# Performance work log

Measured on AMD Instinct MI355X. Metric: run time of the kernel, lower is better.

## Reference

```python
import jax, jax.numpy as jnp
import numpy as np

B, D_IMG, D_TXT, E = 4096, 768, 768, 512
LAMBDA_CMP = 1.0
EPS = 1e-10


def setup_inputs() -> dict:
    key = jax.random.key(0)
    k1, k2, k3, k4, k5 = jax.random.split(key, 5)
    return {
        "images": jax.random.normal(k1, (B, D_IMG), dtype=jnp.float32),
        "texts": jax.random.normal(k2, (B, D_TXT), dtype=jnp.float32),
        "labels": jax.random.randint(k3, (B,), 0, 1000, dtype=jnp.int32),
        "W_img": jax.random.normal(k4, (D_IMG, E), dtype=jnp.float32) / np.sqrt(D_IMG),
        "W_txt": jax.random.normal(k5, (D_TXT, E), dtype=jnp.float32) / np.sqrt(D_TXT),
        "logit_scale": jnp.asarray(np.log(1.0 / 0.07), dtype=jnp.float32),
    }


def reference(images, texts, labels, W_img, W_txt, logit_scale):
    # CLIP-style encoders: linear project + L2 normalize
    img = images @ W_img
    txt = texts @ W_txt
    img = img / jnp.linalg.norm(img, axis=-1, keepdims=True)
    txt = txt / jnp.linalg.norm(txt, axis=-1, keepdims=True)
    logits = jnp.exp(logit_scale) * (img @ txt.T)  # [B, B]

    b = logits.shape[0]
    rows = jnp.arange(b)
    logp = jax.nn.log_softmax(logits, axis=-1)
    clip_loss = -jnp.mean(logp[rows, labels])

    probs = jnp.exp(logp)                # softmax probs [B, B]
    p_yi = probs[rows, labels]           # [B]
    # columns j whose label differs from sample i's label AND prob exceeds p_yi
    diff_label = labels[None, :] != labels[:, None]           # [B, B]
    mask = diff_label & (probs > p_yi[:, None])               # [B, B]
    denom = jnp.sum(jnp.where(mask, probs, 0.0), axis=1)      # [B]
    has_any = jnp.any(mask, axis=1)
    cmp_loss = jnp.sum(jnp.where(has_any, p_yi / (denom + EPS), 0.0)) / b

    return clip_loss + LAMBDA_CMP * cmp_loss
```

## Files before the change

### kernel.cpp

```cpp
#include <hip/hip_runtime.h>
#include <stdint.h>

#define BATCH 4096
#define DDIM  768
#define EDIM  512
#define NSPLIT 16
#define LOG2E 1.44269504088896340736f

using short8  = __attribute__((ext_vector_type(8))) short;
using float4v = __attribute__((ext_vector_type(4))) float;

__device__ __forceinline__ unsigned short f2bf(float x) {
    union { float f; uint32_t u; } v; v.f = x;
    uint32_t u = v.u;
    u += 0x7FFFu + ((u >> 16) & 1u);
    return (unsigned short)(u >> 16);
}
__device__ __forceinline__ float bf2f(unsigned short h) {
    union { uint32_t u; float f; } v; v.u = ((uint32_t)h) << 16;
    return v.f;
}

__device__ __forceinline__ void gl2lds16(const void* g, void* l) {
    __builtin_amdgcn_global_load_lds(
        (const __attribute__((address_space(1))) void*)g,
        (__attribute__((address_space(3))) void*)l, 16, 0, 0);
}

__global__ void prep(const float* __restrict__ images, const float* __restrict__ texts,
                     const float* __restrict__ W_img, const float* __restrict__ W_txt,
                     unsigned short* __restrict__ img_bf, unsigned short* __restrict__ txt_bf,
                     unsigned short* __restrict__ wt_img, unsigned short* __restrict__ wt_txt) {
    __shared__ float tile[32][33];
    int bid = blockIdx.x;
    if (bid < 6144) {
        int which = bid >= 3072;
        int i = (bid - (which ? 3072 : 0)) * 256 + threadIdx.x;
        const float* in = which ? texts : images;
        unsigned short* out = which ? txt_bf : img_bf;
        float4 v = ((const float4*)in)[i];
        ushort4 o;
        o.x = f2bf(v.x); o.y = f2bf(v.y); o.z = f2bf(v.z); o.w = f2bf(v.w);
        ((ushort4*)out)[i] = o;
        return;
    }
    int tb = bid - 6144;
    int which = tb >= 384;
    if (which) tb -= 384;
    const float* W = which ? W_txt : W_img;
    unsigned short* Wt = which ? wt_txt : wt_img;
    int n0 = (tb & 15) * 32, k0 = (tb >> 4) * 32;
    int tid = threadIdx.x;
    for (int p = 0; p < 4; ++p) {
        int e = tid + p * 256; int lr = e >> 5, lc = e & 31;
        tile[lc][lr] = W[(size_t)(k0 + lr) * EDIM + n0 + lc];
    }
    __syncthreads();
    for (int p = 0; p < 4; ++p) {
        int e = tid + p * 256; int lr = e >> 5, lc = e & 31;
        Wt[(size_t)(n0 + lr) * DDIM + k0 + lc] = f2bf(tile[lr][lc]);
    }
}

__global__ __launch_bounds__(256) void gemm_nt(const unsigned short* __restrict__ Aimg,
                                               const unsigned short* __restrict__ Atxt,
                                               const unsigned short* __restrict__ Bimg,
                                               const unsigned short* __restrict__ Btxt,
                                               unsigned short* __restrict__ Cimg,
                                               unsigned short* __restrict__ Ctxt) {
    const unsigned short* A  = blockIdx.z ? Atxt : Aimg;
    const unsigned short* Bm = blockIdx.z ? Btxt : Bimg;
    unsigned short* C        = blockIdx.z ? Ctxt : Cimg;
    __shared__ __align__(16) unsigned short As[2][128 * 64];
    __shared__ __align__(16) unsigned short Bs[2][64 * 64];
    int tid = threadIdx.x;
    int wave = tid >> 6, lane = tid & 63;
    int q = lane >> 4, r = lane & 15;
    int m0 = blockIdx.x * 128, n0 = blockIdx.y * 64;
    int sw = (r >> 1) & 3;

    const unsigned short* gsA[4];
    unsigned short* lsA[4];
    for (int i = 0; i < 4; ++i) {
        int u = i * 256 + tid;
        int kc2 = u >> 9, row = (u >> 2) & 127, kq = u & 3;
        int kq2 = kq ^ ((row >> 1) & 3);
        gsA[i] = &A[(size_t)(m0 + row) * DDIM + kc2 * 32 + kq2 * 8];
        lsA[i] = &As[0][u * 8];
    }
    const unsigned short* gsB[2];
    unsigned short* lsB[2];
    for (int i = 0; i < 2; ++i) {
        int u = i * 256 + tid;
        int kc2 = u >> 8, row = (u >> 2) & 63, kq = u & 3;
        int kq2 = kq ^ ((row >> 1) & 3);
        gsB[i] = &Bm[(size_t)(n0 + row) * DDIM + kc2 * 32 + kq2 * 8];
        lsB[i] = &Bs[0][u * 8];
    }

    float4v acc[2][4];
    for (int a = 0; a < 2; ++a)
        for (int t = 0; t < 4; ++t) acc[a][t] = (float4v){0.f, 0.f, 0.f, 0.f};

    for (int i = 0; i < 4; ++i) gl2lds16(gsA[i], lsA[i]);
    for (int i = 0; i < 2; ++i) gl2lds16(gsB[i], lsB[i]);
    __syncthreads();

    for (int it = 0; it < DDIM / 64; ++it) {
        int b = it & 1;
        if (it < DDIM / 64 - 1) {
            int k0 = (it + 1) * 64;
            for (int i = 0; i < 4; ++i) gl2lds16(gsA[i] + k0, lsA[i] + (b ^ 1) * (128 * 64));
            for (int i = 0; i < 2; ++i) gl2lds16(gsB[i] + k0, lsB[i] + (b ^ 1) * (64 * 64));
        }
        for (int kc2 = 0; kc2 < 2; ++kc2) {
            short8 a0 = *(const short8*)&As[b][kc2 * 4096 + (wave * 32 + r) * 32 + (q ^ sw) * 8];
            short8 a1 = *(const short8*)&As[b][kc2 * 4096 + (wave * 32 + 16 + r) * 32 + (q ^ sw) * 8];
            for (int t = 0; t < 4; ++t) {
                short8 bfr = *(const short8*)&Bs[b][kc2 * 2048 + (t * 16 + r) * 32 + (q ^ sw) * 8];
                acc[0][t] = __builtin_amdgcn_mfma_f32_16x16x32_bf16(a0, bfr, acc[0][t], 0, 0, 0);
                acc[1][t] = __builtin_amdgcn_mfma_f32_16x16x32_bf16(a1, bfr, acc[1][t], 0, 0, 0);
            }
        }
        __syncthreads();
    }
    for (int rg = 0; rg < 2; ++rg)
        for (int t = 0; t < 4; ++t)
            for (int g = 0; g < 4; ++g)
                C[(size_t)(m0 + wave * 32 + rg * 16 + q * 4 + g) * EDIM + n0 + t * 16 + r] =
                    f2bf(acc[rg][t][g]);
}

__global__ void norm_rows(unsigned short* __restrict__ Pa, unsigned short* __restrict__ Pb) {
    unsigned short* P = blockIdx.y ? Pb : Pa;
    int wave = threadIdx.x >> 6, lane = threadIdx.x & 63;
    int row = blockIdx.x * 4 + wave;
    unsigned short* p = &P[(size_t)row * 512 + lane * 8];
    union { unsigned short us[8]; uint4 u4; } v;
    v.u4 = *(const uint4*)p;
    float f[8], s = 0.f;
    for (int j = 0; j < 8; ++j) { f[j] = bf2f(v.us[j]); s += f[j] * f[j]; }
    for (int off = 1; off < 64; off <<= 1) s += __shfl_xor(s, off);
    float rn = rsqrtf(s);
    for (int j = 0; j < 8; ++j) v.us[j] = f2bf(f[j] * rn);
    *(uint4*)p = v.u4;
}

__global__ void tdot(const unsigned short* __restrict__ img, const unsigned short* __restrict__ txt,
                     const int* __restrict__ labels, float* __restrict__ tout) {
    int wave = threadIdx.x >> 6, lane = threadIdx.x & 63;
    int row = blockIdx.x * 4 + wave;
    int lab = labels[row];
    union { unsigned short us[8]; uint4 u4; } a, b;
    a.u4 = *(const uint4*)&img[(size_t)row * 512 + lane * 8];
    b.u4 = *(const uint4*)&txt[(size_t)lab * 512 + lane * 8];
    float s = 0.f;
    for (int j = 0; j < 8; ++j) s += bf2f(a.us[j]) * bf2f(b.us[j]);
    for (int off = 1; off < 64; off <<= 1) s += __shfl_xor(s, off);
    if (lane == 0) tout[row] = s;
}

__global__ __launch_bounds__(512) void flash_pass(
    const unsigned short* __restrict__ img, const unsigned short* __restrict__ txt,
    const int* __restrict__ labels, const float* __restrict__ tvals,
    const float* __restrict__ ls,
    float* __restrict__ lP, float* __restrict__ dP) {
    __shared__ __align__(16) unsigned short Bs[2][16384];
    int tid = threadIdx.x;
    int wave = tid >> 6, lane = tid & 63;
    int q = lane >> 4, r = lane & 15;
    int split = blockIdx.x;
    int row0 = blockIdx.y * 128 + wave * 16;
    float alpha = expf(ls[0]);
    float c1 = alpha * LOG2E;

    int srow = (tid >> 2) & 63, kcb = tid >> 8, skp = tid & 3;
    int skp2 = skp ^ ((srow >> 1) & 3);
    int sw = (r >> 1) & 3;

    const unsigned short* gB0 = &txt[(size_t)(split * 256 + srow) * 512 + kcb * 32 + skp2 * 8];
    unsigned short* ld0 = &Bs[0][0] + (size_t)tid * 8;

    for (int i = 0; i < 4; ++i) gl2lds16(gB0 + i * 64, ld0 + i * 4096);

    short8 af[16];
    for (int kc = 0; kc < 16; ++kc)
        af[kc] = *(const short8*)&img[(size_t)(row0 + r) * 512 + kc * 32 + q * 8];

    int labr[4]; float tr[4];
    for (int g = 0; g < 4; ++g) {
        int rw = row0 + q * 4 + g;
        labr[g] = labels[rw];
        tr[g] = tvals[rw];
    }
    float l[4] = {0.f, 0.f, 0.f, 0.f}, d[4] = {0.f, 0.f, 0.f, 0.f};
    float4v acc[4];
    for (int t = 0; t < 4; ++t) acc[t] = (float4v){0.f, 0.f, 0.f, 0.f};

    __syncthreads();

    for (int s = 0; s < 8; ++s) {
        int buf = s & 1, h = s & 1;
        if (s < 7) {
            int sn = s + 1;
            const unsigned short* g = gB0 + (sn >> 1) * (64 * 512) + (sn & 1) * 256;
            unsigned short* ld = ld0 + (sn & 1) * 16384;
            for (int i = 0; i < 4; ++i) gl2lds16(g + i * 64, ld + i * 4096);
        }
        for (int kc = 0; kc < 8; ++kc) {
            short8 a = af[h * 8 + kc];
            for (int t = 0; t < 4; ++t) {
                short8 bfr = *(const short8*)&Bs[buf][(kc * 64 + t * 16 + r) * 32 + (q ^ sw) * 8];
                acc[t] = __builtin_amdgcn_mfma_f32_16x16x32_bf16(a, bfr, acc[t], 0, 0, 0);
            }
        }
        if (h == 1) {
            int colbase = split * 256 + (s >> 1) * 64;
            for (int t = 0; t < 4; ++t) {
                int lc = labels[colbase + t * 16 + r];
                for (int g = 0; g < 4; ++g) {
                    float a = acc[t][g];
                    float p = exp2f(fmaf(a, c1, -c1));
                    l[g] += p;
                    d[g] += ((a > tr[g]) && (lc != labr[g])) ? p : 0.f;
                }
            }
            for (int t = 0; t < 4; ++t) acc[t] = (float4v){0.f, 0.f, 0.f, 0.f};
        }
        __syncthreads();
    }
    for (int g = 0; g < 4; ++g) {
        float lv = l[g], dv = d[g];
        for (int off = 1; off < 16; off <<= 1) {
            lv += __shfl_xor(lv, off);
            dv += __shfl_xor(dv, off);
        }
        if (r == 0) {
            int rw = row0 + q * 4 + g;
            lP[(size_t)rw * NSPLIT + split] = lv;
            dP[(size_t)rw * NSPLIT + split] = dv;
        }
    }
}

__global__ void combine(const float* __restrict__ lP, const float* __restrict__ dP,
                        const float* __restrict__ tvals, const float* __restrict__ ls,
                        float* __restrict__ out) {
    int row = blockIdx.x * 256 + threadIdx.x;
    float alpha = expf(ls[0]);
    float L = 0.f, D = 0.f;
    for (int s = 0; s < NSPLIT; ++s) {
        L += lP[(size_t)row * NSPLIT + s];
        D += dP[(size_t)row * NSPLIT + s];
    }
    float tm = alpha * (tvals[row] - 1.0f);
    float clip = logf(L) - tm;
    float py = expf(tm) / L;
    float cmp = (D > 0.f) ? py / (D / L + 1e-10f) : 0.f;
    float v = clip + cmp;
    for (int off = 1; off < 64; off <<= 1) v += __shfl_xor(v, off);
    __shared__ float w4[4];
    int wave = threadIdx.x >> 6, lane = threadIdx.x & 63;
    if (lane == 0) w4[wave] = v;
    __syncthreads();
    if (threadIdx.x == 0)
        atomicAdd(out, (w4[0] + w4[1] + w4[2] + w4[3]) * (1.0f / BATCH));
}

extern "C" void kernel_launch(void* const* d_in, const int* in_sizes, int n_in,
                              void* d_out, int out_size, void* d_ws, size_t ws_size,
                              hipStream_t stream) {
    const float* images = (const float*)d_in[0];
    const float* texts  = (const float*)d_in[1];
    const int*   labels = (const int*)d_in[2];
    const float* W_img  = (const float*)d_in[3];
    const float* W_txt  = (const float*)d_in[4];
    const float* lscale = (const float*)d_in[5];
    float* out = (float*)d_out;

    char* ws = (char*)d_ws;
    unsigned short* img_bf = (unsigned short*)(ws + 0);
    unsigned short* txt_bf = (unsigned short*)(ws + 6291456);
    unsigned short* wt_img = (unsigned short*)(ws + 12582912);
    unsigned short* wt_txt = (unsigned short*)(ws + 13369344);
    unsigned short* proj_i = (unsigned short*)(ws + 14155776);
    unsigned short* proj_t = (unsigned short*)(ws + 18350080);
    float*          lP     = (float*)(ws + 0);
    float*          dP     = (float*)(ws + 262144);
    float*          tvals  = (float*)(ws + 524288);

    hipMemsetAsync(out, 0, sizeof(float), stream);
    prep<<<6912, 256, 0, stream>>>(images, texts, W_img, W_txt, img_bf, txt_bf, wt_img, wt_txt);
    gemm_nt<<<dim3(BATCH / 128, EDIM / 64, 2), 256, 0, stream>>>(img_bf, txt_bf, wt_img, wt_txt,
                                                                 proj_i, proj_t);
    norm_rows<<<dim3(BATCH / 4, 2), 256, 0, stream>>>(proj_i, proj_t);
    tdot<<<BATCH / 4, 256, 0, stream>>>(proj_i, proj_t, labels, tvals);
    flash_pass<<<dim3(NSPLIT, BATCH / 128), 512, 0, stream>>>(proj_i, proj_t, labels, tvals,
                                                              lscale, lP, dP);
    combine<<<16, 256, 0, stream>>>(lP, dP, tvals, lscale, out);
}
```

Before: 136.5 us.

## Give each flash_pass wave two 16-row tiles and halve block threads

The flash_pass kernel now runs 4 waves per block instead of 8, and each wave covers 32 image rows as two 16-row MFMA subtiles. Every B fragment read from LDS feeds two MFMAs, which halves LDS read traffic per MFMA. The txt tile loader is reorganised so 256 threads issue 8 global-to-LDS copies each. The cost is more registers per wave (doubled A fragments and accumulators) and fewer waves available to hide latency, which launch_bounds(256,2) tries to balance.

```diff
diff --git a/kernel.cpp b/kernel.cpp
--- a/kernel.cpp
+++ b/kernel.cpp
@@ -160,7 +160,7 @@
     if (lane == 0) tout[row] = s;
 }
 
-__global__ __launch_bounds__(512) void flash_pass(
+__global__ __launch_bounds__(256, 2) void flash_pass(
     const unsigned short* __restrict__ img, const unsigned short* __restrict__ txt,
     const int* __restrict__ labels, const float* __restrict__ tvals,
     const float* __restrict__ ls,
@@ -170,32 +170,36 @@
     int wave = tid >> 6, lane = tid & 63;
     int q = lane >> 4, r = lane & 15;
     int split = blockIdx.x;
-    int row0 = blockIdx.y * 128 + wave * 16;
+    int row0 = blockIdx.y * 128 + wave * 32;
     float alpha = expf(ls[0]);
     float c1 = alpha * LOG2E;
 
-    int srow = (tid >> 2) & 63, kcb = tid >> 8, skp = tid & 3;
+    int srow = (tid >> 2) & 63, skp = tid & 3;
     int skp2 = skp ^ ((srow >> 1) & 3);
     int sw = (r >> 1) & 3;
 
-    const unsigned short* gB0 = &txt[(size_t)(split * 256 + srow) * 512 + kcb * 32 + skp2 * 8];
+    const unsigned short* gB0 = &txt[(size_t)(split * 256 + srow) * 512 + skp2 * 8];
     unsigned short* ld0 = &Bs[0][0] + (size_t)tid * 8;
 
-    for (int i = 0; i < 4; ++i) gl2lds16(gB0 + i * 64, ld0 + i * 4096);
-
-    short8 af[16];
-    for (int kc = 0; kc < 16; ++kc)
-        af[kc] = *(const short8*)&img[(size_t)(row0 + r) * 512 + kc * 32 + q * 8];
-
-    int labr[4]; float tr[4];
-    for (int g = 0; g < 4; ++g) {
-        int rw = row0 + q * 4 + g;
-        labr[g] = labels[rw];
-        tr[g] = tvals[rw];
-    }
-    float l[4] = {0.f, 0.f, 0.f, 0.f}, d[4] = {0.f, 0.f, 0.f, 0.f};
-    float4v acc[4];
-    for (int t = 0; t < 4; ++t) acc[t] = (float4v){0.f, 0.f, 0.f, 0.f};
+    for (int i = 0; i < 8; ++i) gl2lds16(gB0 + i * 32, ld0 + i * 2048);
+
+    short8 af[2][16];
+    for (int st = 0; st < 2; ++st)
+        for (int kc = 0; kc < 16; ++kc)
+            af[st][kc] = *(const short8*)&img[(size_t)(row0 + st * 16 + r) * 512 + kc * 32 + q * 8];
+
+    int labr[2][4]; float tr[2][4];
+    for (int st = 0; st < 2; ++st)
+        for (int g = 0; g < 4; ++g) {
+            int rw = row0 + st * 16 + q * 4 + g;
+            labr[st][g] = labels[rw];
+            tr[st][g] = tvals[rw];
+        }
+    float l[2][4] = {{0.f, 0.f, 0.f, 0.f}, {0.f, 0.f, 0.f, 0.f}};
+    float d[2][4] = {{0.f, 0.f, 0.f, 0.f}, {0.f, 0.f, 0.f, 0.f}};
+    float4v acc[2][4];
+    for (int st = 0; st < 2; ++st)
+        for (int t = 0; t < 4; ++t) acc[st][t] = (float4v){0.f, 0.f, 0.f, 0.f};
 
     __syncthreads();
 
@@ -205,42 +209,46 @@
             int sn = s + 1;
             const unsigned short* g = gB0 + (sn >> 1) * (64 * 512) + (sn & 1) * 256;
             unsigned short* ld = ld0 + (sn & 1) * 16384;
-            for (int i = 0; i < 4; ++i) gl2lds16(g + i * 64, ld + i * 4096);
+            for (int i = 0; i < 8; ++i) gl2lds16(g + i * 32, ld + i * 2048);
         }
         for (int kc = 0; kc < 8; ++kc) {
-            short8 a = af[h * 8 + kc];
+            short8 a0 = af[0][h * 8 + kc];
+            short8 a1 = af[1][h * 8 + kc];
             for (int t = 0; t < 4; ++t) {
                 short8 bfr = *(const short8*)&Bs[buf][(kc * 64 + t * 16 + r) * 32 + (q ^ sw) * 8];
-                acc[t] = __builtin_amdgcn_mfma_f32_16x16x32_bf16(a, bfr, acc[t], 0, 0, 0);
+                acc[0][t] = __builtin_amdgcn_mfma_f32_16x16x32_bf16(a0, bfr, acc[0][t], 0, 0, 0);
+                acc[1][t] = __builtin_amdgcn_mfma_f32_16x16x32_bf16(a1, bfr, acc[1][t], 0, 0, 0);
             }
         }
         if (h == 1) {
             int colbase = split * 256 + (s >> 1) * 64;
             for (int t = 0; t < 4; ++t) {
                 int lc = labels[colbase + t * 16 + r];
-                for (int g = 0; g < 4; ++g) {
-                    float a = acc[t][g];
-                    float p = exp2f(fmaf(a, c1, -c1));
-                    l[g] += p;
-                    d[g] += ((a > tr[g]) && (lc != labr[g])) ? p : 0.f;
-                }
-            }
-            for (int t = 0; t < 4; ++t) acc[t] = (float4v){0.f, 0.f, 0.f, 0.f};
+                for (int st = 0; st < 2; ++st)
+                    for (int g = 0; g < 4; ++g) {
+                        float a = acc[st][t][g];
+                        float p = exp2f(fmaf(a, c1, -c1));
+                        l[st][g] += p;
+                        d[st][g] += ((a > tr[st][g]) && (lc != labr[st][g])) ? p : 0.f;
+                    }
+                for (int st = 0; st < 2; ++st) acc[st][t] = (float4v){0.f, 0.f, 0.f, 0.f};
+            }
         }
         __syncthreads();
     }
-    for (int g = 0; g < 4; ++g) {
-        float lv = l[g], dv = d[g];
-        for (int off = 1; off < 16; off <<= 1) {
-            lv += __shfl_xor(lv, off);
-            dv += __shfl_xor(dv, off);
-        }
-        if (r == 0) {
-            int rw = row0 + q * 4 + g;
-            lP[(size_t)rw * NSPLIT + split] = lv;
-            dP[(size_t)rw * NSPLIT + split] = dv;
-        }
-    }
+    for (int st = 0; st < 2; ++st)
+        for (int g = 0; g < 4; ++g) {
+            float lv = l[st][g], dv = d[st][g];
+            for (int off = 1; off < 16; off <<= 1) {
+                lv += __shfl_xor(lv, off);
+                dv += __shfl_xor(dv, off);
+            }
+            if (r == 0) {
+                int rw = row0 + st * 16 + q * 4 + g;
+                lP[(size_t)rw * NSPLIT + split] = lv;
+                dP[(size_t)rw * NSPLIT + split] = dv;
+            }
+        }
 }
 
 __global__ void combine(const float* __restrict__ lP, const float* __restrict__ dP,
@@ -295,7 +303,7 @@
                                                                  proj_i, proj_t);
     norm_rows<<<dim3(BATCH / 4, 2), 256, 0, stream>>>(proj_i, proj_t);
     tdot<<<BATCH / 4, 256, 0, stream>>>(proj_i, proj_t, labels, tvals);
-    flash_pass<<<dim3(NSPLIT, BATCH / 128), 512, 0, stream>>>(proj_i, proj_t, labels, tvals,
+    flash_pass<<<dim3(NSPLIT, BATCH / 128), 256, 0, stream>>>(proj_i, proj_t, labels, tvals,
                                                               lscale, lP, dP);
     combine<<<16, 256, 0, stream>>>(lP, dP, tvals, lscale, out);
 }
```

Result: slower. 157.8 us (+15.6%).

## Restructure similarity pass into 128x128 tiled GEMM with per-tile partial sums

Applied to the files above, without the earlier changes.

The flash pass changes from one block per 128 rows sweeping 256 columns, with the A operand held in registers and only 4 accumulators per wave, to a classic 128x128 output tile. Each block double-buffers both A and B K-slices into LDS, and each wave computes a 64x64 sub-tile (4x4 MFMA accumulators). The softmax and mask partial sums are then reduced per 64-column chunk, which raises the partial count per row from 16 to 64. The aim is more MFMA work per LDS fragment load and a larger grid (1024 blocks). The cost is extra A traffic through LDS and a larger partial buffer that combine must read.

```diff
diff --git a/kernel.cpp b/kernel.cpp
--- a/kernel.cpp
+++ b/kernel.cpp
@@ -4,7 +4,7 @@
 #define BATCH 4096
 #define DDIM  768
 #define EDIM  512
-#define NSPLIT 16
+#define NS    64
 #define LOG2E 1.44269504088896340736f
 
 using short8  = __attribute__((ext_vector_type(8))) short;
@@ -160,85 +160,106 @@
     if (lane == 0) tout[row] = s;
 }
 
-__global__ __launch_bounds__(512) void flash_pass(
+__global__ __launch_bounds__(256) void flash_pass(
     const unsigned short* __restrict__ img, const unsigned short* __restrict__ txt,
     const int* __restrict__ labels, const float* __restrict__ tvals,
     const float* __restrict__ ls,
     float* __restrict__ lP, float* __restrict__ dP) {
-    __shared__ __align__(16) unsigned short Bs[2][16384];
+    __shared__ __align__(16) unsigned short As[2][128 * 64];
+    __shared__ __align__(16) unsigned short Bs[2][128 * 64];
     int tid = threadIdx.x;
     int wave = tid >> 6, lane = tid & 63;
+    int wr = wave >> 1, wc = wave & 1;
     int q = lane >> 4, r = lane & 15;
-    int split = blockIdx.x;
-    int row0 = blockIdx.y * 128 + wave * 16;
+    int n0 = blockIdx.x * 128;
+    int m0 = blockIdx.y * 128;
     float alpha = expf(ls[0]);
     float c1 = alpha * LOG2E;
-
-    int srow = (tid >> 2) & 63, kcb = tid >> 8, skp = tid & 3;
-    int skp2 = skp ^ ((srow >> 1) & 3);
     int sw = (r >> 1) & 3;
 
-    const unsigned short* gB0 = &txt[(size_t)(split * 256 + srow) * 512 + kcb * 32 + skp2 * 8];
-    unsigned short* ld0 = &Bs[0][0] + (size_t)tid * 8;
-
-    for (int i = 0; i < 4; ++i) gl2lds16(gB0 + i * 64, ld0 + i * 4096);
-
-    short8 af[16];
-    for (int kc = 0; kc < 16; ++kc)
-        af[kc] = *(const short8*)&img[(size_t)(row0 + r) * 512 + kc * 32 + q * 8];
-
-    int labr[4]; float tr[4];
-    for (int g = 0; g < 4; ++g) {
-        int rw = row0 + q * 4 + g;
-        labr[g] = labels[rw];
-        tr[g] = tvals[rw];
-    }
-    float l[4] = {0.f, 0.f, 0.f, 0.f}, d[4] = {0.f, 0.f, 0.f, 0.f};
-    float4v acc[4];
-    for (int t = 0; t < 4; ++t) acc[t] = (float4v){0.f, 0.f, 0.f, 0.f};
-
+    const unsigned short* gsA[4]; const unsigned short* gsB[4];
+    unsigned short *lsA[4], *lsB[4];
+    for (int i = 0; i < 4; ++i) {
+        int u = i * 256 + tid;
+        int kc2 = u >> 9, row = (u >> 2) & 127, kq = u & 3;
+        int kq2 = kq ^ ((row >> 1) & 3);
+        gsA[i] = &img[(size_t)(m0 + row) * 512 + kc2 * 32 + kq2 * 8];
+        gsB[i] = &txt[(size_t)(n0 + row) * 512 + kc2 * 32 + kq2 * 8];
+        lsA[i] = &As[0][u * 8];
+        lsB[i] = &Bs[0][u * 8];
+    }
+
+    float4v acc[4][4];
+    #pragma unroll
+    for (int st = 0; st < 4; ++st)
+        #pragma unroll
+        for (int cf = 0; cf < 4; ++cf) acc[st][cf] = (float4v){0.f, 0.f, 0.f, 0.f};
+
+    for (int i = 0; i < 4; ++i) gl2lds16(gsA[i], lsA[i]);
+    for (int i = 0; i < 4; ++i) gl2lds16(gsB[i], lsB[i]);
     __syncthreads();
 
-    for (int s = 0; s < 8; ++s) {
-        int buf = s & 1, h = s & 1;
-        if (s < 7) {
-            int sn = s + 1;
-            const unsigned short* g = gB0 + (sn >> 1) * (64 * 512) + (sn & 1) * 256;
-            unsigned short* ld = ld0 + (sn & 1) * 16384;
-            for (int i = 0; i < 4; ++i) gl2lds16(g + i * 64, ld + i * 4096);
-        }
-        for (int kc = 0; kc < 8; ++kc) {
-            short8 a = af[h * 8 + kc];
-            for (int t = 0; t < 4; ++t) {
-                short8 bfr = *(const short8*)&Bs[buf][(kc * 64 + t * 16 + r) * 32 + (q ^ sw) * 8];
-                acc[t] = __builtin_amdgcn_mfma_f32_16x16x32_bf16(a, bfr, acc[t], 0, 0, 0);
+    for (int it = 0; it < 8; ++it) {
+        int b = it & 1;
+        if (it < 7) {
+            int k0 = (it + 1) * 64;
+            for (int i = 0; i < 4; ++i) gl2lds16(gsA[i] + k0, lsA[i] + (b ^ 1) * (128 * 64));
+            for (int i = 0; i < 4; ++i) gl2lds16(gsB[i] + k0, lsB[i] + (b ^ 1) * (128 * 64));
+        }
+        #pragma unroll
+        for (int kc2 = 0; kc2 < 2; ++kc2) {
+            short8 av[4], bv[4];
+            #pragma unroll
+            for (int st = 0; st < 4; ++st)
+                av[st] = *(const short8*)&As[b][kc2 * 4096 + (wr * 64 + st * 16 + r) * 32 + (q ^ sw) * 8];
+            #pragma unroll
+            for (int cf = 0; cf < 4; ++cf)
+                bv[cf] = *(const short8*)&Bs[b][kc2 * 4096 + (wc * 64 + cf * 16 + r) * 32 + (q ^ sw) * 8];
+            #pragma unroll
+            for (int st = 0; st < 4; ++st)
+                #pragma unroll
+                for (int cf = 0; cf < 4; ++cf)
+                    acc[st][cf] = __builtin_amdgcn_mfma_f32_16x16x32_bf16(av[st], bv[cf],
+                                                                          acc[st][cf], 0, 0, 0);
+        }
+        __syncthreads();
+    }
+
+    int lc[4];
+    #pragma unroll
+    for (int cf = 0; cf < 4; ++cf) lc[cf] = labels[n0 + wc * 64 + cf * 16 + r];
+    int cb = blockIdx.x * 2 + wc;
+    #pragma unroll
+    for (int st = 0; st < 4; ++st) {
+        int labr[4]; float tr[4];
+        #pragma unroll
+        for (int g = 0; g < 4; ++g) {
+            int rw = m0 + wr * 64 + st * 16 + q * 4 + g;
+            labr[g] = labels[rw];
+            tr[g] = tvals[rw];
+        }
+        float l4[4] = {0.f, 0.f, 0.f, 0.f}, d4[4] = {0.f, 0.f, 0.f, 0.f};
+        #pragma unroll
+        for (int cf = 0; cf < 4; ++cf)
+            #pragma unroll
+            for (int g = 0; g < 4; ++g) {
+                float a = acc[st][cf][g];
+                float p = exp2f(fmaf(a, c1, -c1));
+                l4[g] += p;
+                d4[g] += ((a > tr[g]) && (lc[cf] != labr[g])) ? p : 0.f;
             }
-        }
-        if (h == 1) {
-            int colbase = split * 256 + (s >> 1) * 64;
-            for (int t = 0; t < 4; ++t) {
-                int lc = labels[colbase + t * 16 + r];
-                for (int g = 0; g < 4; ++g) {
-                    float a = acc[t][g];
-                    float p = exp2f(fmaf(a, c1, -c1));
-                    l[g] += p;
-                    d[g] += ((a > tr[g]) && (lc != labr[g])) ? p : 0.f;
-                }
+        #pragma unroll
+        for (int g = 0; g < 4; ++g) {
+            float lv = l4[g], dv = d4[g];
+            for (int off = 1; off < 16; off <<= 1) {
+                lv += __shfl_xor(lv, off);
+                dv += __shfl_xor(dv, off);
             }
-            for (int t = 0; t < 4; ++t) acc[t] = (float4v){0.f, 0.f, 0.f, 0.f};
-        }
-        __syncthreads();
-    }
-    for (int g = 0; g < 4; ++g) {
-        float lv = l[g], dv = d[g];
-        for (int off = 1; off < 16; off <<= 1) {
-            lv += __shfl_xor(lv, off);
-            dv += __shfl_xor(dv, off);
-        }
-        if (r == 0) {
-            int rw = row0 + q * 4 + g;
-            lP[(size_t)rw * NSPLIT + split] = lv;
-            dP[(size_t)rw * NSPLIT + split] = dv;
+            if (r == 0) {
+                int rw = m0 + wr * 64 + st * 16 + q * 4 + g;
+                lP[(size_t)rw * NS + cb] = lv;
+                dP[(size_t)rw * NS + cb] = dv;
+            }
         }
     }
 }
@@ -249,9 +270,9 @@
     int row = blockIdx.x * 256 + threadIdx.x;
     float alpha = expf(ls[0]);
     float L = 0.f, D = 0.f;
-    for (int s = 0; s < NSPLIT; ++s) {
-        L += lP[(size_t)row * NSPLIT + s];
-        D += dP[(size_t)row * NSPLIT + s];
+    for (int s = 0; s < NS; ++s) {
+        L += lP[(size_t)row * NS + s];
+        D += dP[(size_t)row * NS + s];
     }
     float tm = alpha * (tvals[row] - 1.0f);
     float clip = logf(L) - tm;
@@ -286,8 +307,8 @@
     unsigned short* proj_i = (unsigned short*)(ws + 14155776);
     unsigned short* proj_t = (unsigned short*)(ws + 18350080);
     float*          lP     = (float*)(ws + 0);
-    float*          dP     = (float*)(ws + 262144);
-    float*          tvals  = (float*)(ws + 524288);
+    float*          dP     = (float*)(ws + 1048576);
+    float*          tvals  = (float*)(ws + 2097152);
 
     hipMemsetAsync(out, 0, sizeof(float), stream);
     prep<<<6912, 256, 0, stream>>>(images, texts, W_img, W_txt, img_bf, txt_bf, wt_img, wt_txt);
@@ -295,7 +316,7 @@
                                                                  proj_i, proj_t);
     norm_rows<<<dim3(BATCH / 4, 2), 256, 0, stream>>>(proj_i, proj_t);
     tdot<<<BATCH / 4, 256, 0, stream>>>(proj_i, proj_t, labels, tvals);
-    flash_pass<<<dim3(NSPLIT, BATCH / 128), 512, 0, stream>>>(proj_i, proj_t, labels, tvals,
-                                                              lscale, lP, dP);
+    flash_pass<<<dim3(BATCH / 128, BATCH / 128), 256, 0, stream>>>(proj_i, proj_t, labels, tvals,
+                                                                   lscale, lP, dP);
     combine<<<16, 256, 0, stream>>>(lP, dP, tvals, lscale, out);
 }
```

Result: slower. 141.0 us (+3.3%).
